# Optimization experiments

Hardware: AMD Instinct MI355X
Metric: run time of the kernel (lower is better)

The kernel has to match this reference:

```python
import jax, jax.numpy as jnp
import numpy as np

D = 1024
H = 16
DH = D // H
MAX_TYPES = 256
B, L = 8, 1024
EPS = 1e-5


def setup_inputs() -> dict:
    key = jax.random.key(0)
    ks = jax.random.split(key, 16)
    s = 0.02
    return {
        'type_ids': jax.random.randint(ks[0], (B, L), 0, MAX_TYPES),
        'values': jax.random.normal(ks[1], (B, L, 1), jnp.float32),
        'deltas': jax.random.uniform(ks[2], (B, L, 1), jnp.float32),
        'type_emb': jax.random.normal(ks[3], (MAX_TYPES, D), jnp.float32) * s,
        'Wv': jax.random.normal(ks[4], (D, 1), jnp.float32) * s,
        'bv': jnp.zeros((D,), jnp.float32),
        'Wt': jax.random.normal(ks[5], (D, 1), jnp.float32) * s,
        'bt': jnp.zeros((D,), jnp.float32),
        'Win': jax.random.normal(ks[6], (3 * D, D), jnp.float32) * s,
        'bin': jnp.zeros((3 * D,), jnp.float32),
        'Wout': jax.random.normal(ks[7], (D, D), jnp.float32) * s,
        'bout': jnp.zeros((D,), jnp.float32),
        'W1': jax.random.normal(ks[8], (D, D), jnp.float32) * s,
        'b1': jnp.zeros((D,), jnp.float32),
        'W2': jax.random.normal(ks[9], (D, D), jnp.float32) * s,
        'b2': jnp.zeros((D,), jnp.float32),
        'gamma': jnp.ones((D,), jnp.float32),
        'beta': jnp.zeros((D,), jnp.float32),
    }


def _ln(x, gamma, beta):
    mu = jnp.mean(x, axis=-1, keepdims=True)
    var = jnp.mean(jnp.square(x - mu), axis=-1, keepdims=True)
    return (x - mu) * jax.lax.rsqrt(var + EPS) * gamma + beta


def reference(type_ids, values, deltas, type_emb, Wv, bv, Wt, bt,
              Win, bin, Wout, bout, W1, b1, W2, b2, gamma, beta):
    # fused embedding: type lookup + value/time linear projections
    h = type_emb[type_ids] + values @ Wv.T + bv + deltas @ Wt.T + bt  # [B,L,D]
    b, l, d = h.shape
    # multi-head self-attention (explicit weights path, need_weights=True)
    qkv = h @ Win.T + bin  # [B,L,3D]
    q, k, v = jnp.split(qkv, 3, axis=-1)
    q = q.reshape(b, l, H, DH)
    k = k.reshape(b, l, H, DH)
    v = v.reshape(b, l, H, DH)
    scale = 1.0 / jnp.sqrt(jnp.asarray(DH, h.dtype))
    scores = jnp.einsum('blhd,bmhd->bhlm', q, k) * scale  # [B,H,L,L]
    w = jax.nn.softmax(scores, axis=-1)
    attn = jnp.einsum('bhlm,bmhd->blhd', w, v).reshape(b, l, d)
    attn_out = attn @ Wout.T + bout
    h2 = _ln(h + attn_out, gamma, beta)
    ff = jax.nn.relu(h2 @ W1.T + b1) @ W2.T + b2
    h3 = _ln(h2 + ff, gamma, beta)
    pooled = h3.mean(axis=1)  # [B,D]
    attn_tokens = w.mean(axis=1).mean(axis=2)  # mean over heads, then keys -> [B,L]
    return pooled, attn_tokens
```

## Files before the change

kernel.cpp:

```cpp
#include <hip/hip_runtime.h>
#include <hip/hip_bf16.h>


#define Dm 1024
#define Hh 16
#define Bb 8
#define Ll 1024
#define Mm 8192
#define LNEPS 1e-5f

typedef __attribute__((ext_vector_type(8))) short s16x8;
typedef __attribute__((ext_vector_type(4))) short s16x4;
typedef __attribute__((ext_vector_type(4))) float f32x4;

using bf16 = __hip_bfloat16;

__device__ __forceinline__ short f2bs(float f) {
  return __builtin_bit_cast(short, __float2bfloat16(f));
}

__device__ __forceinline__ unsigned cvtpk(float lo, float hi) {
  unsigned r;
  asm("v_cvt_pk_bf16_f32 %0, %1, %2" : "=v"(r) : "v"(lo), "v"(hi));
  return r;
}

__device__ __forceinline__ void gload16(const void* g, void* l) {
  __builtin_amdgcn_global_load_lds(
      (__attribute__((address_space(1))) void*)g,
      (__attribute__((address_space(3))) void*)l, 16, 0, 0);
}

__global__ __launch_bounds__(256) void k_f2b(const float* __restrict__ x, bf16* __restrict__ y)
{
  const size_t i = ((size_t)blockIdx.x * 256 + threadIdx.x) * 4;
  const float4 v = *(const float4*)&x[i];
  s16x4 o;
  o[0] = f2bs(v.x); o[1] = f2bs(v.y); o[2] = f2bs(v.z); o[3] = f2bs(v.w);
  *(s16x4*)&y[i] = o;
}

__global__ __launch_bounds__(256) void k_embed(
    const int* __restrict__ tids, const float* __restrict__ vals, const float* __restrict__ dels,
    const float* __restrict__ temb, const float* __restrict__ Wv, const float* __restrict__ bv,
    const float* __restrict__ Wt, const float* __restrict__ bt,
    float* __restrict__ hf, bf16* __restrict__ hb)
{
  const int row = blockIdx.x;
  const int ty = tids[row];
  const float v = vals[row], dl = dels[row];
  const int d0 = threadIdx.x * 4;
  const float4 e  = *(const float4*)&temb[(size_t)ty * Dm + d0];
  const float4 wv = *(const float4*)&Wv[d0];
  const float4 c1 = *(const float4*)&bv[d0];
  const float4 wt = *(const float4*)&Wt[d0];
  const float4 c2 = *(const float4*)&bt[d0];
  float4 h;
  h.x = e.x + v * wv.x + c1.x + dl * wt.x + c2.x;
  h.y = e.y + v * wv.y + c1.y + dl * wt.y + c2.y;
  h.z = e.z + v * wv.z + c1.z + dl * wt.z + c2.z;
  h.w = e.w + v * wv.w + c1.w + dl * wt.w + c2.w;
  *(float4*)&hf[(size_t)row * Dm + d0] = h;
  s16x4 o;
  o[0] = f2bs(h.x); o[1] = f2bs(h.y); o[2] = f2bs(h.z); o[3] = f2bs(h.w);
  *(s16x4*)((short*)hb + (size_t)row * Dm + d0) = o;
}

template<bool RELU, bool OUTF, bool OUTB, bool RES>
__global__ __launch_bounds__(256) void k_gemm_bt(
    const bf16* __restrict__ A, const bf16* __restrict__ Bt,
    const float* __restrict__ bias, const float* __restrict__ res,
    float* __restrict__ outF, bf16* __restrict__ outB, const int N, const int K)
{
  __shared__ __attribute__((aligned(16))) short lA[4096];
  __shared__ __attribute__((aligned(16))) short lB[4096];
  const int tid = threadIdx.x, lane = tid & 63, wave = tid >> 6;
  const int wr = wave >> 1, wc = wave & 1;
  const int l15 = lane & 15, lg = lane >> 4;
  const size_t bm = blockIdx.x, bn = blockIdx.y;
  f32x4 acc[4][4] = {};
  const int srow = tid >> 2, scol = (tid & 3) << 3;
  const bf16* ga = A  + (bm * 128 + srow) * (size_t)K + scol;
  const bf16* gb = Bt + (bn * 128 + srow) * (size_t)K + scol;
  for (int k0 = 0; k0 < K; k0 += 32) {
    gload16(ga + k0,                  &lA[tid * 8]);
    gload16(ga + k0 + (size_t)64 * K, &lA[2048 + tid * 8]);
    gload16(gb + k0,                  &lB[tid * 8]);
    gload16(gb + k0 + (size_t)64 * K, &lB[2048 + tid * 8]);
    __syncthreads();
    s16x8 fa[4], fb[4];
#pragma unroll
    for (int m = 0; m < 4; ++m)
      fa[m] = *(const s16x8*)&lA[(wr * 64 + m * 16 + l15) * 32 + lg * 8];
#pragma unroll
    for (int n = 0; n < 4; ++n)
      fb[n] = *(const s16x8*)&lB[(wc * 64 + n * 16 + l15) * 32 + lg * 8];
    __builtin_amdgcn_s_setprio(1);
#pragma unroll
    for (int m = 0; m < 4; ++m)
#pragma unroll
      for (int n = 0; n < 4; ++n)
        acc[m][n] = __builtin_amdgcn_mfma_f32_16x16x32_bf16(fa[m], fb[n], acc[m][n], 0, 0, 0);
    __builtin_amdgcn_s_setprio(0);
    __syncthreads();
  }
#pragma unroll
  for (int n = 0; n < 4; ++n) {
    const int col = (int)bn * 128 + wc * 64 + n * 16 + l15;
    const float bc = bias[col];
#pragma unroll
    for (int m = 0; m < 4; ++m) {
#pragma unroll
      for (int i = 0; i < 4; ++i) {
        const size_t row = bm * 128 + wr * 64 + m * 16 + lg * 4 + i;
        float v = acc[m][n][i] + bc;
        if constexpr (RES)  v += res[row * N + col];
        if constexpr (RELU) v = fmaxf(v, 0.f);
        if constexpr (OUTF) outF[row * N + col] = v;
        if constexpr (OUTB) outB[row * N + col] = __float2bfloat16(v);
      }
    }
  }
}

__global__ __launch_bounds__(256) void k_vt(const bf16* __restrict__ qkv, bf16* __restrict__ vt)
{
  const int bh = blockIdx.x, lc = blockIdx.y;
  const int b = bh >> 4, h = bh & 15;
  __shared__ short tile[64][72];
  const int r = threadIdx.x >> 2;
  const int c0 = (threadIdx.x & 3) << 4;
  const short* src = (const short*)qkv + ((size_t)(b * Ll + lc * 64 + r)) * 3072 + 2048 + h * 64 + c0;
  const s16x8 x0 = *(const s16x8*)src;
  const s16x8 x1 = *(const s16x8*)(src + 8);
#pragma unroll
  for (int j = 0; j < 8; ++j) { tile[r][c0 + j] = x0[j]; tile[r][c0 + 8 + j] = x1[j]; }
  __syncthreads();
  s16x8 y0, y1;
#pragma unroll
  for (int j = 0; j < 8; ++j) { y0[j] = tile[c0 + j][r]; y1[j] = tile[c0 + 8 + j][r]; }
  short* dst = (short*)vt + ((size_t)(bh * 64 + r)) * Ll + lc * 64 + c0;
  *(s16x8*)dst = y0;
  *(s16x8*)(dst + 8) = y1;
}

__global__ __launch_bounds__(256) void k_attn(
    const bf16* __restrict__ qkv, const bf16* __restrict__ vt, bf16* __restrict__ attnb)
{
  const int bh = blockIdx.x;
  const int qb = blockIdx.y;
  const int b = bh >> 4, h = bh & 15;
  __shared__ __attribute__((aligned(16))) short lK[4096];
  __shared__ __attribute__((aligned(16))) short lV[4096];
  __shared__ __attribute__((aligned(16))) short lP[8192];
  const int tid = threadIdx.x, lane = tid & 63, wave = tid >> 6;
  const int l15 = lane & 15, lg = lane >> 4;
  const int qrow = wave * 32;
  const int l7 = l15 & 7;

  s16x8 qf[2][2];
#pragma unroll
  for (int mq = 0; mq < 2; ++mq)
#pragma unroll
    for (int ks = 0; ks < 2; ++ks)
      qf[mq][ks] = *(const s16x8*)((const short*)qkv +
          ((size_t)(b * Ll + qb * 128 + qrow + mq * 16 + l15)) * 3072 + h * 64 + ks * 32 + lg * 8);

  f32x4 o[2][4] = {};
  float rs[2] = {0.f, 0.f};

  const int sr = tid >> 3;
  const int sc = tid & 7;
  const int swz = sc ^ (sr & 7);

  for (int mc = 0; mc < 16; ++mc) {
    __syncthreads();
    {
      const bf16* gk = qkv + ((size_t)(b * Ll + mc * 64 + sr)) * 3072 + 1024 + h * 64 + swz * 8;
      gload16(gk,                     &lK[tid * 8]);
      gload16(gk + (size_t)32 * 3072, &lK[2048 + tid * 8]);
      const bf16* gv = vt + ((size_t)(bh * 64 + sr)) * Ll + mc * 64 + swz * 8;
      gload16(gv,                   &lV[tid * 8]);
      gload16(gv + (size_t)32 * Ll, &lV[2048 + tid * 8]);
    }
    __syncthreads();

    f32x4 st[2][4] = {};
    __builtin_amdgcn_s_setprio(1);
#pragma unroll
    for (int ks = 0; ks < 2; ++ks) {
#pragma unroll
      for (int n = 0; n < 4; ++n) {
        const int kr = n * 16 + l15;
        const s16x8 kf = *(const s16x8*)&lK[kr * 64 + (((ks * 4 + lg) ^ l7) << 3)];
        st[0][n] = __builtin_amdgcn_mfma_f32_16x16x32_bf16(kf, qf[0][ks], st[0][n], 0, 0, 0);
        st[1][n] = __builtin_amdgcn_mfma_f32_16x16x32_bf16(kf, qf[1][ks], st[1][n], 0, 0, 0);
      }
    }
    __builtin_amdgcn_s_setprio(0);

#pragma unroll
    for (int mq = 0; mq < 2; ++mq) {
      const int qr = qrow + mq * 16 + l15;
      short* prow = &lP[qr * 64];
      float loc = 0.f;
#pragma unroll
      for (int n = 0; n < 4; ++n) {
        const float e0 = __expf(st[mq][n][0] * 0.125f);
        const float e1 = __expf(st[mq][n][1] * 0.125f);
        const float e2 = __expf(st[mq][n][2] * 0.125f);
        const float e3 = __expf(st[mq][n][3] * 0.125f);
        loc += (e0 + e1) + (e2 + e3);
        const unsigned c0 = cvtpk(e0, e1);
        const unsigned c1 = cvtpk(e2, e3);
        const int col0 = n * 16 + lg * 4;
        const int scol = ((((col0 >> 3) ^ (qr & 7)) << 3) | (col0 & 7));
        *(unsigned*)&prow[scol]     = c0;
        *(unsigned*)&prow[scol + 2] = c1;
      }
      rs[mq] += loc;
    }

    __builtin_amdgcn_s_setprio(1);
#pragma unroll
    for (int ks = 0; ks < 2; ++ks) {
      s16x8 pa[2];
#pragma unroll
      for (int mq = 0; mq < 2; ++mq) {
        const int qr = qrow + mq * 16 + l15;
        pa[mq] = *(const s16x8*)&lP[qr * 64 + (((ks * 4 + lg) ^ (qr & 7)) << 3)];
      }
#pragma unroll
      for (int dn = 0; dn < 4; ++dn) {
        const int vr = dn * 16 + l15;
        const s16x8 vf = *(const s16x8*)&lV[vr * 64 + (((ks * 4 + lg) ^ l7) << 3)];
        o[0][dn] = __builtin_amdgcn_mfma_f32_16x16x32_bf16(pa[0], vf, o[0][dn], 0, 0, 0);
        o[1][dn] = __builtin_amdgcn_mfma_f32_16x16x32_bf16(pa[1], vf, o[1][dn], 0, 0, 0);
      }
    }
    __builtin_amdgcn_s_setprio(0);
  }

#pragma unroll
  for (int mq = 0; mq < 2; ++mq) {
    rs[mq] += __shfl_xor(rs[mq], 16);
    rs[mq] += __shfl_xor(rs[mq], 32);
  }
#pragma unroll
  for (int mq = 0; mq < 2; ++mq) {
    float inv[4];
#pragma unroll
    for (int i = 0; i < 4; ++i)
      inv[i] = 1.f / __shfl(rs[mq], lg * 4 + i);
#pragma unroll
    for (int dn = 0; dn < 4; ++dn) {
#pragma unroll
      for (int i = 0; i < 4; ++i) {
        const int q = qb * 128 + qrow + mq * 16 + lg * 4 + i;
        attnb[((size_t)(b * Ll + q)) * Dm + h * 64 + dn * 16 + l15] =
            __float2bfloat16(o[mq][dn][i] * inv[i]);
      }
    }
  }
}

template<bool WB>
__global__ __launch_bounds__(256) void k_ln(const float* __restrict__ x,
    const float* __restrict__ gamma, const float* __restrict__ beta,
    float* __restrict__ yf, bf16* __restrict__ yb)
{
  const size_t row = blockIdx.x;
  const int d0 = threadIdx.x * 4;
  const float4 xv = *(const float4*)&x[row * Dm + d0];
  float s  = xv.x + xv.y + xv.z + xv.w;
  float ss = xv.x * xv.x + xv.y * xv.y + xv.z * xv.z + xv.w * xv.w;
#pragma unroll
  for (int m = 1; m < 64; m <<= 1) { s += __shfl_xor(s, m); ss += __shfl_xor(ss, m); }
  __shared__ float red[8];
  const int wv = threadIdx.x >> 6;
  if ((threadIdx.x & 63) == 0) { red[wv] = s; red[4 + wv] = ss; }
  __syncthreads();
  s  = red[0] + red[1] + red[2] + red[3];
  ss = red[4] + red[5] + red[6] + red[7];
  const float mu = s * (1.f / Dm);
  const float rstd = rsqrtf(ss * (1.f / Dm) - mu * mu + LNEPS);
  const float4 g  = *(const float4*)&gamma[d0];
  const float4 be = *(const float4*)&beta[d0];
  float4 y;
  y.x = (xv.x - mu) * rstd * g.x + be.x;
  y.y = (xv.y - mu) * rstd * g.y + be.y;
  y.z = (xv.z - mu) * rstd * g.z + be.z;
  y.w = (xv.w - mu) * rstd * g.w + be.w;
  *(float4*)&yf[row * Dm + d0] = y;
  if constexpr (WB) {
    s16x4 o;
    o[0] = f2bs(y.x); o[1] = f2bs(y.y); o[2] = f2bs(y.z); o[3] = f2bs(y.w);
    *(s16x4*)((short*)yb + row * Dm + d0) = o;
  }
}

__global__ __launch_bounds__(256) void k_pool_part(const float* __restrict__ h3, float* __restrict__ part)
{
  const int b = blockIdx.x, lcn = blockIdx.y, dz = blockIdx.z;
  const int d = dz * 256 + threadIdx.x;
  float s = 0.f;
#pragma unroll 4
  for (int l = 0; l < 64; ++l)
    s += h3[((size_t)(b * Ll + lcn * 64 + l)) * Dm + d];
  part[((size_t)(b * 16 + lcn)) * Dm + d] = s;
}

__global__ __launch_bounds__(256) void k_pool_fin(const float* __restrict__ part, float* __restrict__ out)
{
  const int b = blockIdx.x;
  const int d = blockIdx.y * 256 + threadIdx.x;
  float s = 0.f;
#pragma unroll
  for (int c = 0; c < 16; ++c) s += part[((size_t)(b * 16 + c)) * Dm + d];
  out[b * Dm + d] = s * (1.f / Ll);
  out[(size_t)Mm + b * Dm + d] = 1.f / Ll;
}

extern "C" void kernel_launch(void* const* d_in, const int* in_sizes, int n_in,
                              void* d_out, int out_size, void* d_ws, size_t ws_size,
                              hipStream_t stream) {
  const int*   tids  = (const int*)  d_in[0];
  const float* vals  = (const float*)d_in[1];
  const float* dels  = (const float*)d_in[2];
  const float* temb  = (const float*)d_in[3];
  const float* Wv    = (const float*)d_in[4];
  const float* bv    = (const float*)d_in[5];
  const float* Wt    = (const float*)d_in[6];
  const float* bt    = (const float*)d_in[7];
  const float* Win   = (const float*)d_in[8];
  const float* bin   = (const float*)d_in[9];
  const float* Wout  = (const float*)d_in[10];
  const float* bout  = (const float*)d_in[11];
  const float* W1    = (const float*)d_in[12];
  const float* b1    = (const float*)d_in[13];
  const float* W2    = (const float*)d_in[14];
  const float* b2    = (const float*)d_in[15];
  const float* gamma = (const float*)d_in[16];
  const float* beta  = (const float*)d_in[17];
  float* out = (float*)d_out;

  char* w = (char*)d_ws;
  const size_t MB = 1ull << 20;
  float* hf    = (float*)(w + 0);
  bf16*  hb    = (bf16*) (w + 32 * MB);
  bf16*  qkv   = (bf16*) (w + 48 * MB);
  bf16*  vtb   = (bf16*) (w + 96 * MB);
  bf16*  attnb = (bf16*) (w + 112 * MB);
  float* x1    = (float*)(w + 48 * MB);
  float* h2f   = (float*)(w + 80 * MB);
  bf16*  h2b   = (bf16*) (w + 32 * MB);
  bf16*  ff1   = (bf16*) (w + 112 * MB);
  float* x2    = (float*)(w + 0);
  float* h3    = (float*)(w + 48 * MB);
  bf16*  WinB  = (bf16*) (w + 129 * MB);
  bf16*  WoutB = (bf16*) (w + 135 * MB);
  bf16*  W1B   = (bf16*) (w + 137 * MB);
  bf16*  W2B   = (bf16*) (w + 139 * MB);
  float* part  = (float*)(w + 141 * MB);

  k_f2b<<<3072, 256, 0, stream>>>(Win,  WinB);
  k_f2b<<<1024, 256, 0, stream>>>(Wout, WoutB);
  k_f2b<<<1024, 256, 0, stream>>>(W1,   W1B);
  k_f2b<<<1024, 256, 0, stream>>>(W2,   W2B);

  k_embed<<<Mm, 256, 0, stream>>>(tids, vals, dels, temb, Wv, bv, Wt, bt, hf, hb);

  k_gemm_bt<false, false, true, false><<<dim3(64, 24), 256, 0, stream>>>(
      hb, WinB, bin, nullptr, nullptr, qkv, 3072, 1024);

  k_vt<<<dim3(128, 16), 256, 0, stream>>>(qkv, vtb);
  k_attn<<<dim3(128, 8), 256, 0, stream>>>(qkv, vtb, attnb);

  k_gemm_bt<false, true, false, true><<<dim3(64, 8), 256, 0, stream>>>(
      attnb, WoutB, bout, hf, x1, nullptr, 1024, 1024);

  k_ln<true><<<Mm, 256, 0, stream>>>(x1, gamma, beta, h2f, h2b);

  k_gemm_bt<true, false, true, false><<<dim3(64, 8), 256, 0, stream>>>(
      h2b, W1B, b1, nullptr, nullptr, ff1, 1024, 1024);

  k_gemm_bt<false, true, false, true><<<dim3(64, 8), 256, 0, stream>>>(
      ff1, W2B, b2, h2f, x2, nullptr, 1024, 1024);

  k_ln<false><<<Mm, 256, 0, stream>>>(x2, gamma, beta, h3, nullptr);

  k_pool_part<<<dim3(8, 16, 4), 256, 0, stream>>>(h3, part);
  k_pool_fin<<<dim3(8, 4), 256, 0, stream>>>(part, out);
}
```

Measured before the change: 273.2 us.

## Replace GEMM with 8-wave 128x256 tile, double-buffered swizzled LDS pipeline

```diff
diff --git a/kernel.cpp b/kernel.cpp
--- a/kernel.cpp
+++ b/kernel.cpp
@@ -67,52 +67,148 @@
 }
 
 template<bool RELU, bool OUTF, bool OUTB, bool RES>
-__global__ __launch_bounds__(256) void k_gemm_bt(
+__global__ __launch_bounds__(512) void k_gemm8(
     const bf16* __restrict__ A, const bf16* __restrict__ Bt,
     const float* __restrict__ bias, const float* __restrict__ res,
     float* __restrict__ outF, bf16* __restrict__ outB, const int N, const int K)
 {
-  __shared__ __attribute__((aligned(16))) short lA[4096];
-  __shared__ __attribute__((aligned(16))) short lB[4096];
+  __shared__ __attribute__((aligned(16))) short lds[49152];
   const int tid = threadIdx.x, lane = tid & 63, wave = tid >> 6;
-  const int wr = wave >> 1, wc = wave & 1;
-  const int l15 = lane & 15, lg = lane >> 4;
-  const size_t bm = blockIdx.x, bn = blockIdx.y;
+  const int wr = wave >> 2, wc = wave & 3;
+  const int l15 = lane & 15, lg = (lane >> 4) & 3;
+  const int bm = blockIdx.x, bn = blockIdx.y;
+  const int NT = K >> 6;
+
+  const int rl = tid >> 3;
+  const int swz = ((tid & 7) ^ (rl & 7)) * 8;
+  const bf16* aSrc = A  + (size_t)(bm * 128 + rl) * K + swz;
+  const bf16* bSrc = Bt + (size_t)(bn * 256 + rl) * K + swz;
+
   f32x4 acc[4][4] = {};
-  const int srow = tid >> 2, scol = (tid & 3) << 3;
-  const bf16* ga = A  + (bm * 128 + srow) * (size_t)K + scol;
-  const bf16* gb = Bt + (bn * 128 + srow) * (size_t)K + scol;
-  for (int k0 = 0; k0 < K; k0 += 32) {
-    gload16(ga + k0,                  &lA[tid * 8]);
-    gload16(ga + k0 + (size_t)64 * K, &lA[2048 + tid * 8]);
-    gload16(gb + k0,                  &lB[tid * 8]);
-    gload16(gb + k0 + (size_t)64 * K, &lB[2048 + tid * 8]);
-    __syncthreads();
-    s16x8 fa[4], fb[4];
-#pragma unroll
-    for (int m = 0; m < 4; ++m)
-      fa[m] = *(const s16x8*)&lA[(wr * 64 + m * 16 + l15) * 32 + lg * 8];
-#pragma unroll
-    for (int n = 0; n < 4; ++n)
-      fb[n] = *(const s16x8*)&lB[(wc * 64 + n * 16 + l15) * 32 + lg * 8];
-    __builtin_amdgcn_s_setprio(1);
-#pragma unroll
-    for (int m = 0; m < 4; ++m)
-#pragma unroll
-      for (int n = 0; n < 4; ++n)
-        acc[m][n] = __builtin_amdgcn_mfma_f32_16x16x32_bf16(fa[m], fb[n], acc[m][n], 0, 0, 0);
-    __builtin_amdgcn_s_setprio(0);
-    __syncthreads();
-  }
+
+  auto stageA = [&](int t, int h) {
+    gload16(aSrc + (size_t)h * 64 * K + t * 64,
+            &lds[(t & 1) * 24576 + h * 4096 + tid * 8]);
+  };
+  auto stageB = [&](int t, int h) {
+    gload16(bSrc + (size_t)h * 128 * K + t * 64,
+            &lds[(t & 1) * 24576 + 8192 + h * 8192 + tid * 8]);
+    gload16(bSrc + (size_t)(h * 128 + 64) * K + t * 64,
+            &lds[(t & 1) * 24576 + 8192 + h * 8192 + 4096 + tid * 8]);
+  };
+
+  stageA(0, 0); stageA(0, 1); stageB(0, 0); stageB(0, 1);
+  if (NT > 1) { stageA(1, 0); stageA(1, 1); }
+  asm volatile("s_waitcnt vmcnt(2)" ::: "memory");
+  __builtin_amdgcn_sched_barrier(0);
+  __builtin_amdgcn_s_barrier();
+
+  for (int t = 0; t < NT; ++t) {
+    const int cb = (t & 1) * 24576;
+    s16x8 fa[4][2], fb[2][2];
+
+#pragma unroll
+    for (int m = 0; m < 2; ++m)
+#pragma unroll
+      for (int ks = 0; ks < 2; ++ks) {
+        const int row = wr * 64 + m * 16 + l15;
+        fa[m][ks] = *(const s16x8*)&lds[cb + row * 64 + (((ks * 4 + lg) ^ (row & 7)) << 3)];
+      }
+#pragma unroll
+    for (int n = 0; n < 2; ++n)
+#pragma unroll
+      for (int ks = 0; ks < 2; ++ks) {
+        const int row = wc * 64 + n * 16 + l15;
+        fb[n][ks] = *(const s16x8*)&lds[cb + 8192 + row * 64 + (((ks * 4 + lg) ^ (row & 7)) << 3)];
+      }
+    if (t + 1 < NT) stageB(t + 1, 0);
+    __builtin_amdgcn_s_barrier();
+    asm volatile("s_waitcnt lgkmcnt(0)" ::: "memory");
+    __builtin_amdgcn_sched_barrier(0);
+    __builtin_amdgcn_s_setprio(1);
+#pragma unroll
+    for (int m = 0; m < 2; ++m)
+#pragma unroll
+      for (int n = 0; n < 2; ++n)
+#pragma unroll
+        for (int ks = 0; ks < 2; ++ks)
+          acc[m][n] = __builtin_amdgcn_mfma_f32_16x16x32_bf16(fa[m][ks], fb[n][ks], acc[m][n], 0, 0, 0);
+    __builtin_amdgcn_s_setprio(0);
+    __builtin_amdgcn_s_barrier();
+
+#pragma unroll
+    for (int m = 0; m < 2; ++m)
+#pragma unroll
+      for (int ks = 0; ks < 2; ++ks) {
+        const int row = wr * 64 + (2 + m) * 16 + l15;
+        fa[2 + m][ks] = *(const s16x8*)&lds[cb + row * 64 + (((ks * 4 + lg) ^ (row & 7)) << 3)];
+      }
+    if (t + 1 < NT) stageB(t + 1, 1);
+    __builtin_amdgcn_s_barrier();
+    asm volatile("s_waitcnt lgkmcnt(0)" ::: "memory");
+    __builtin_amdgcn_sched_barrier(0);
+    __builtin_amdgcn_s_setprio(1);
+#pragma unroll
+    for (int m = 0; m < 2; ++m)
+#pragma unroll
+      for (int n = 0; n < 2; ++n)
+#pragma unroll
+        for (int ks = 0; ks < 2; ++ks)
+          acc[2 + m][n] = __builtin_amdgcn_mfma_f32_16x16x32_bf16(fa[2 + m][ks], fb[n][ks], acc[2 + m][n], 0, 0, 0);
+    __builtin_amdgcn_s_setprio(0);
+    __builtin_amdgcn_s_barrier();
+
+#pragma unroll
+    for (int n = 0; n < 2; ++n)
+#pragma unroll
+      for (int ks = 0; ks < 2; ++ks) {
+        const int row = wc * 64 + (2 + n) * 16 + l15;
+        fb[n][ks] = *(const s16x8*)&lds[cb + 8192 + row * 64 + (((ks * 4 + lg) ^ (row & 7)) << 3)];
+      }
+    if (t + 2 < NT) stageA(t + 2, 0);
+    __builtin_amdgcn_s_barrier();
+    asm volatile("s_waitcnt lgkmcnt(0)" ::: "memory");
+    __builtin_amdgcn_sched_barrier(0);
+    __builtin_amdgcn_s_setprio(1);
+#pragma unroll
+    for (int m = 0; m < 2; ++m)
+#pragma unroll
+      for (int n = 0; n < 2; ++n)
+#pragma unroll
+        for (int ks = 0; ks < 2; ++ks)
+          acc[m][2 + n] = __builtin_amdgcn_mfma_f32_16x16x32_bf16(fa[m][ks], fb[n][ks], acc[m][2 + n], 0, 0, 0);
+    __builtin_amdgcn_s_setprio(0);
+    __builtin_amdgcn_s_barrier();
+
+    if (t + 2 < NT) stageA(t + 2, 1);
+    __builtin_amdgcn_s_barrier();
+    __builtin_amdgcn_s_setprio(1);
+#pragma unroll
+    for (int m = 0; m < 2; ++m)
+#pragma unroll
+      for (int n = 0; n < 2; ++n)
+#pragma unroll
+        for (int ks = 0; ks < 2; ++ks)
+          acc[2 + m][2 + n] = __builtin_amdgcn_mfma_f32_16x16x32_bf16(fa[2 + m][ks], fb[n][ks], acc[2 + m][2 + n], 0, 0, 0);
+    __builtin_amdgcn_s_setprio(0);
+
+    if (t + 1 < NT) {
+      if (t + 2 < NT) asm volatile("s_waitcnt vmcnt(2)" ::: "memory");
+      else            asm volatile("s_waitcnt vmcnt(0)" ::: "memory");
+      __builtin_amdgcn_sched_barrier(0);
+      __builtin_amdgcn_s_barrier();
+    }
+  }
+
 #pragma unroll
   for (int n = 0; n < 4; ++n) {
-    const int col = (int)bn * 128 + wc * 64 + n * 16 + l15;
+    const int col = bn * 256 + wc * 64 + n * 16 + l15;
     const float bc = bias[col];
 #pragma unroll
     for (int m = 0; m < 4; ++m) {
 #pragma unroll
       for (int i = 0; i < 4; ++i) {
-        const size_t row = bm * 128 + wr * 64 + m * 16 + lg * 4 + i;
+        const size_t row = (size_t)bm * 128 + wr * 64 + m * 16 + lg * 4 + i;
         float v = acc[m][n][i] + bc;
         if constexpr (RES)  v += res[row * N + col];
         if constexpr (RELU) v = fmaxf(v, 0.f);
@@ -170,8 +266,7 @@
   float rs[2] = {0.f, 0.f};
 
   const int sr = tid >> 3;
-  const int sc = tid & 7;
-  const int swz = sc ^ (sr & 7);
+  const int swz = (tid & 7) ^ (sr & 7);
 
   for (int mc = 0; mc < 16; ++mc) {
     __syncthreads();
@@ -370,21 +465,21 @@
 
   k_embed<<<Mm, 256, 0, stream>>>(tids, vals, dels, temb, Wv, bv, Wt, bt, hf, hb);
 
-  k_gemm_bt<false, false, true, false><<<dim3(64, 24), 256, 0, stream>>>(
+  k_gemm8<false, false, true, false><<<dim3(64, 12), 512, 0, stream>>>(
       hb, WinB, bin, nullptr, nullptr, qkv, 3072, 1024);
 
   k_vt<<<dim3(128, 16), 256, 0, stream>>>(qkv, vtb);
   k_attn<<<dim3(128, 8), 256, 0, stream>>>(qkv, vtb, attnb);
 
-  k_gemm_bt<false, true, false, true><<<dim3(64, 8), 256, 0, stream>>>(
+  k_gemm8<false, true, false, true><<<dim3(64, 4), 512, 0, stream>>>(
       attnb, WoutB, bout, hf, x1, nullptr, 1024, 1024);
 
   k_ln<true><<<Mm, 256, 0, stream>>>(x1, gamma, beta, h2f, h2b);
 
-  k_gemm_bt<true, false, true, false><<<dim3(64, 8), 256, 0, stream>>>(
+  k_gemm8<true, false, true, false><<<dim3(64, 4), 512, 0, stream>>>(
       h2b, W1B, b1, nullptr, nullptr, ff1, 1024, 1024);
 
-  k_gemm_bt<false, true, false, true><<<dim3(64, 8), 256, 0, stream>>>(
+  k_gemm8<false, true, false, true><<<dim3(64, 4), 512, 0, stream>>>(
       ff1, W2B, b2, h2f, x2, nullptr, 1024, 1024);
 
   k_ln<false><<<Mm, 256, 0, stream>>>(x2, gamma, beta, h3, nullptr);
```

New measurement: 263.6 us. 3.5% less time.
